# Kernel optimization log

Measured on AMD Instinct MI355X. Metric: run time of the kernel, lower is better.

The kernel has to match this reference:

```python
import jax, jax.numpy as jnp
import numpy as np

D = 256

def setup_inputs() -> dict:
    key = jax.random.key(0)
    k1, k2, k3, k4, k5, k6 = jax.random.split(key, 6)
    M, N = 2048, 512
    s = 1.0 / np.sqrt(D)
    return {
        "q_vec": jax.random.normal(k1, (M, D), dtype=jnp.float32),
        "kv": jax.random.normal(k2, (M, N, D), dtype=jnp.float32),
        "wq": jax.random.uniform(k3, (D, D), jnp.float32, -s, s),
        "wk": jax.random.uniform(k4, (D, D), jnp.float32, -s, s),
        "wv": jax.random.uniform(k5, (D, D), jnp.float32, -s, s),
        "wo": (jax.random.uniform(k6, (D, D), jnp.float32, -s, s)),
    }

def reference(q_vec, kv, wq, wk, wv, wo):
    # q_vec: [M, d], kv: [M, N, d]; weights stored torch-style [out, in] -> apply x @ W.T
    d = q_vec.shape[-1]
    q = q_vec @ wq.T                          # [M, d]
    k = jnp.einsum('mnd,ed->mne', kv, wk)     # [M, N, d]
    v = jnp.einsum('mnd,ed->mne', kv, wv)     # [M, N, d]
    logits = jnp.einsum('md,mnd->mn', q, k) / jnp.sqrt(jnp.float32(d))  # [M, N]
    attn = jax.nn.softmax(logits, axis=-1)    # [M, N] (dropout p=0.0 is identity)
    ctx = jnp.einsum('mn,mnd->md', attn, v)   # [M, d]
    out = ctx @ wo.T                          # [M, d]
    return out, attn
```

## Files before the change

kernel.cpp:

```cpp
#include <hip/hip_runtime.h>
#include <math.h>

#define DD 256
#define MM 2048
#define NN 512

typedef float f32x4 __attribute__((ext_vector_type(4)));

__device__ inline f32x4 ld_nt(const f32x4* p) { return __builtin_nontemporal_load(p); }

__global__ void prep_weights(const float* __restrict__ wq, const float* __restrict__ wk,
                             const float* __restrict__ wv, const float* __restrict__ wo,
                             float* __restrict__ W1, float* __restrict__ W2T) {
    __shared__ float sA[DD];
    const int j = threadIdx.x;
    const int b = blockIdx.x;
    if (b < DD) {
        const int d = b;
        sA[j] = wq[j * DD + d];
        __syncthreads();
        float acc = 0.f;
        for (int a = 0; a < DD; ++a) acc = fmaf(sA[a], wk[a * DD + j], acc);
        W1[d * DD + j] = acc * 0.0625f;
    } else {
        const int d = b - DD;
        sA[j] = wv[j * DD + d];
        __syncthreads();
        float acc = 0.f;
        for (int e = 0; e < DD; ++e) acc = fmaf(wo[j * DD + e], sA[e], acc);
        W2T[d * DD + j] = acc;
    }
}

template <int ROWS>
__global__ void rowgemm(const float* __restrict__ X, const float* __restrict__ W,
                        float* __restrict__ Y) {
    __shared__ float sX[ROWS][DD];
    const int j = threadIdx.x;
    const int m0 = blockIdx.x * ROWS;
    for (int r = 0; r < ROWS; ++r) sX[r][j] = X[(size_t)(m0 + r) * DD + j];
    __syncthreads();
    float acc[ROWS];
#pragma unroll
    for (int r = 0; r < ROWS; ++r) acc[r] = 0.f;
    for (int d = 0; d < DD; ++d) {
        const float w = W[d * DD + j];
#pragma unroll
        for (int r = 0; r < ROWS; ++r) acc[r] = fmaf(sX[r][d], w, acc[r]);
    }
    for (int r = 0; r < ROWS; ++r) Y[(size_t)(m0 + r) * DD + j] = acc[r];
}

__global__ __launch_bounds__(256, 4)
void attn_stream(const float* __restrict__ kv, const float* __restrict__ qt,
                 float* __restrict__ c_out, float* __restrict__ attn_out) {
    __shared__ float s_pe[NN];
    __shared__ float s_lw[4];
    __shared__ float s_wc[4][DD];
    __shared__ float s_qt[DD];

    const int m    = blockIdx.x;
    const int tid  = threadIdx.x;
    const int wave = tid >> 6;
    const int lane = tid & 63;
    const int grp  = lane >> 4;
    const int l16  = lane & 15;
    const int nbase = wave * 4 + grp;

    const f32x4* p = (const f32x4*)(kv + (size_t)m * NN * DD) + (size_t)nbase * 64 + l16;
    const int STRIDE = 16 * 64;

    f32x4 a0 = ld_nt(p), a1 = ld_nt(p + 16), a2 = ld_nt(p + 32), a3 = ld_nt(p + 48);

    s_qt[tid] = qt[(size_t)m * DD + tid];
    __syncthreads();

    const f32x4* qt4 = (const f32x4*)s_qt;
    const f32x4 qv0 = qt4[l16];
    const f32x4 qv1 = qt4[l16 + 16];
    const f32x4 qv2 = qt4[l16 + 32];
    const f32x4 qv3 = qt4[l16 + 48];

    f32x4 c0 = (f32x4)0.f, c1 = (f32x4)0.f, c2 = (f32x4)0.f, c3 = (f32x4)0.f;
    float lw = 0.f;

#pragma unroll 2
    for (int it = 0; it < NN / 16; ++it) {
        f32x4 b0, b1, b2, b3;
        if (it + 1 < NN / 16) {
            const f32x4* np = p + (size_t)(it + 1) * STRIDE;
            b0 = ld_nt(np); b1 = ld_nt(np + 16); b2 = ld_nt(np + 32); b3 = ld_nt(np + 48);
        }
        f32x4 t = a0 * qv0 + a1 * qv1 + a2 * qv2 + a3 * qv3;
        float pd = (t[0] + t[1]) + (t[2] + t[3]);
        pd += __shfl_xor(pd, 1);
        pd += __shfl_xor(pd, 2);
        pd += __shfl_xor(pd, 4);
        pd += __shfl_xor(pd, 8);

        const float pe = __expf(pd);
        if (l16 == 0) s_pe[it * 16 + nbase] = pe;
        lw += pe;

        c0 += pe * a0;
        c1 += pe * a1;
        c2 += pe * a2;
        c3 += pe * a3;

        a0 = b0; a1 = b1; a2 = b2; a3 = b3;
    }

#pragma unroll
    for (int i = 0; i < 4; ++i) {
        c0[i] += __shfl_xor(c0[i], 16); c1[i] += __shfl_xor(c1[i], 16);
        c2[i] += __shfl_xor(c2[i], 16); c3[i] += __shfl_xor(c3[i], 16);
        c0[i] += __shfl_xor(c0[i], 32); c1[i] += __shfl_xor(c1[i], 32);
        c2[i] += __shfl_xor(c2[i], 32); c3[i] += __shfl_xor(c3[i], 32);
    }
    lw += __shfl_xor(lw, 16);
    lw += __shfl_xor(lw, 32);

    {
        f32x4* wc4 = (f32x4*)(&s_wc[wave][0]);
        const f32x4 cg = (grp == 0) ? c0 : (grp == 1) ? c1 : (grp == 2) ? c2 : c3;
        wc4[grp * 16 + l16] = cg;
        if (lane == 0) s_lw[wave] = lw;
    }
    __syncthreads();

    const float L = (s_lw[0] + s_lw[1]) + (s_lw[2] + s_lw[3]);
    const float invL = 1.f / L;

    const float cd = ((s_wc[0][tid] + s_wc[1][tid]) + (s_wc[2][tid] + s_wc[3][tid])) * invL;
    c_out[(size_t)m * DD + tid] = cd;

    attn_out[(size_t)m * NN + tid]       = s_pe[tid] * invL;
    attn_out[(size_t)m * NN + tid + 256] = s_pe[tid + 256] * invL;
}

extern "C" void kernel_launch(void* const* d_in, const int* in_sizes, int n_in,
                              void* d_out, int out_size, void* d_ws, size_t ws_size,
                              hipStream_t stream) {
    const float* q_vec = (const float*)d_in[0];
    const float* kv    = (const float*)d_in[1];
    const float* wq    = (const float*)d_in[2];
    const float* wk    = (const float*)d_in[3];
    const float* wv    = (const float*)d_in[4];
    const float* wo    = (const float*)d_in[5];

    float* out  = (float*)d_out;
    float* attn = (float*)d_out + (size_t)MM * DD;

    float* W1  = (float*)d_ws;
    float* W2T = W1 + DD * DD;
    float* qt  = W2T + DD * DD;
    float* cws = qt + (size_t)MM * DD;

    prep_weights<<<2 * DD, DD, 0, stream>>>(wq, wk, wv, wo, W1, W2T);
    rowgemm<16><<<MM / 16, DD, 0, stream>>>(q_vec, W1, qt);
    attn_stream<<<MM, DD, 0, stream>>>(kv, qt, cws, attn);
    rowgemm<16><<<MM / 16, DD, 0, stream>>>(cws, W2T, out);
}
```

Measured before the change: 229.0 us.

## Fuse query and output projections into attention kernel; use packed FP32 FMA

```diff
diff --git a/kernel.cpp b/kernel.cpp
--- a/kernel.cpp
+++ b/kernel.cpp
@@ -6,8 +6,20 @@
 #define NN 512
 
 typedef float f32x4 __attribute__((ext_vector_type(4)));
+typedef float f32x2 __attribute__((ext_vector_type(2)));
 
 __device__ inline f32x4 ld_nt(const f32x4* p) { return __builtin_nontemporal_load(p); }
+
+__device__ inline void pk_fma(f32x2& d, f32x2 a, f32x2 b) {
+    asm("v_pk_fma_f32 %0, %1, %2, %0" : "+v"(d) : "v"(a), "v"(b));
+}
+__device__ inline f32x2 pk_mul(f32x2 a, f32x2 b) {
+    f32x2 d;
+    asm("v_pk_mul_f32 %0, %1, %2" : "=v"(d) : "v"(a), "v"(b));
+    return d;
+}
+__device__ inline f32x2 lo2(f32x4 v) { return __builtin_shufflevector(v, v, 0, 1); }
+__device__ inline f32x2 hi2(f32x4 v) { return __builtin_shufflevector(v, v, 2, 3); }
 
 __global__ void prep_weights(const float* __restrict__ wq, const float* __restrict__ wk,
                              const float* __restrict__ wv, const float* __restrict__ wo,
@@ -32,31 +44,14 @@
     }
 }
 
-template <int ROWS>
-__global__ void rowgemm(const float* __restrict__ X, const float* __restrict__ W,
-                        float* __restrict__ Y) {
-    __shared__ float sX[ROWS][DD];
-    const int j = threadIdx.x;
-    const int m0 = blockIdx.x * ROWS;
-    for (int r = 0; r < ROWS; ++r) sX[r][j] = X[(size_t)(m0 + r) * DD + j];
-    __syncthreads();
-    float acc[ROWS];
-#pragma unroll
-    for (int r = 0; r < ROWS; ++r) acc[r] = 0.f;
-    for (int d = 0; d < DD; ++d) {
-        const float w = W[d * DD + j];
-#pragma unroll
-        for (int r = 0; r < ROWS; ++r) acc[r] = fmaf(sX[r][d], w, acc[r]);
-    }
-    for (int r = 0; r < ROWS; ++r) Y[(size_t)(m0 + r) * DD + j] = acc[r];
-}
-
 __global__ __launch_bounds__(256, 4)
-void attn_stream(const float* __restrict__ kv, const float* __restrict__ qt,
-                 float* __restrict__ c_out, float* __restrict__ attn_out) {
+void attn_fused(const float* __restrict__ q_vec, const float* __restrict__ kv,
+                const float* __restrict__ W1, const float* __restrict__ W2T,
+                float* __restrict__ out, float* __restrict__ attn_out) {
     __shared__ float s_pe[NN];
     __shared__ float s_lw[4];
     __shared__ float s_wc[4][DD];
+    __shared__ float s_q[DD];
     __shared__ float s_qt[DD];
 
     const int m    = blockIdx.x;
@@ -67,22 +62,35 @@
     const int l16  = lane & 15;
     const int nbase = wave * 4 + grp;
 
+    s_q[tid] = q_vec[(size_t)m * DD + tid];
+    __syncthreads();
+    {
+        float a = 0.f;
+#pragma unroll 8
+        for (int d = 0; d < DD; ++d) a = fmaf(s_q[d], W1[d * DD + tid], a);
+        s_qt[tid] = a;
+    }
+    __syncthreads();
+
+    const f32x4* qt4 = (const f32x4*)s_qt;
+    f32x2 qp[8];
+    {
+        const f32x4 q0 = qt4[l16], q1 = qt4[l16 + 16], q2 = qt4[l16 + 32], q3 = qt4[l16 + 48];
+        qp[0] = lo2(q0); qp[1] = hi2(q0);
+        qp[2] = lo2(q1); qp[3] = hi2(q1);
+        qp[4] = lo2(q2); qp[5] = hi2(q2);
+        qp[6] = lo2(q3); qp[7] = hi2(q3);
+    }
+
     const f32x4* p = (const f32x4*)(kv + (size_t)m * NN * DD) + (size_t)nbase * 64 + l16;
     const int STRIDE = 16 * 64;
 
+    f32x2 cp[8];
+#pragma unroll
+    for (int i = 0; i < 8; ++i) cp[i] = (f32x2)0.f;
+    float lw = 0.f;
+
     f32x4 a0 = ld_nt(p), a1 = ld_nt(p + 16), a2 = ld_nt(p + 32), a3 = ld_nt(p + 48);
-
-    s_qt[tid] = qt[(size_t)m * DD + tid];
-    __syncthreads();
-
-    const f32x4* qt4 = (const f32x4*)s_qt;
-    const f32x4 qv0 = qt4[l16];
-    const f32x4 qv1 = qt4[l16 + 16];
-    const f32x4 qv2 = qt4[l16 + 32];
-    const f32x4 qv3 = qt4[l16 + 48];
-
-    f32x4 c0 = (f32x4)0.f, c1 = (f32x4)0.f, c2 = (f32x4)0.f, c3 = (f32x4)0.f;
-    float lw = 0.f;
 
 #pragma unroll 2
     for (int it = 0; it < NN / 16; ++it) {
@@ -91,8 +99,19 @@
             const f32x4* np = p + (size_t)(it + 1) * STRIDE;
             b0 = ld_nt(np); b1 = ld_nt(np + 16); b2 = ld_nt(np + 32); b3 = ld_nt(np + 48);
         }
-        f32x4 t = a0 * qv0 + a1 * qv1 + a2 * qv2 + a3 * qv3;
-        float pd = (t[0] + t[1]) + (t[2] + t[3]);
+
+        const f32x2 ap0 = lo2(a0), ap1 = hi2(a0), ap2 = lo2(a1), ap3 = hi2(a1);
+        const f32x2 ap4 = lo2(a2), ap5 = hi2(a2), ap6 = lo2(a3), ap7 = hi2(a3);
+
+        f32x2 t2 = pk_mul(ap0, qp[0]);
+        pk_fma(t2, ap1, qp[1]);
+        pk_fma(t2, ap2, qp[2]);
+        pk_fma(t2, ap3, qp[3]);
+        pk_fma(t2, ap4, qp[4]);
+        pk_fma(t2, ap5, qp[5]);
+        pk_fma(t2, ap6, qp[6]);
+        pk_fma(t2, ap7, qp[7]);
+        float pd = t2[0] + t2[1];
         pd += __shfl_xor(pd, 1);
         pd += __shfl_xor(pd, 2);
         pd += __shfl_xor(pd, 4);
@@ -102,28 +121,34 @@
         if (l16 == 0) s_pe[it * 16 + nbase] = pe;
         lw += pe;
 
-        c0 += pe * a0;
-        c1 += pe * a1;
-        c2 += pe * a2;
-        c3 += pe * a3;
+        f32x2 pe2; pe2[0] = pe; pe2[1] = pe;
+        pk_fma(cp[0], pe2, ap0);
+        pk_fma(cp[1], pe2, ap1);
+        pk_fma(cp[2], pe2, ap2);
+        pk_fma(cp[3], pe2, ap3);
+        pk_fma(cp[4], pe2, ap4);
+        pk_fma(cp[5], pe2, ap5);
+        pk_fma(cp[6], pe2, ap6);
+        pk_fma(cp[7], pe2, ap7);
 
         a0 = b0; a1 = b1; a2 = b2; a3 = b3;
     }
 
 #pragma unroll
-    for (int i = 0; i < 4; ++i) {
-        c0[i] += __shfl_xor(c0[i], 16); c1[i] += __shfl_xor(c1[i], 16);
-        c2[i] += __shfl_xor(c2[i], 16); c3[i] += __shfl_xor(c3[i], 16);
-        c0[i] += __shfl_xor(c0[i], 32); c1[i] += __shfl_xor(c1[i], 32);
-        c2[i] += __shfl_xor(c2[i], 32); c3[i] += __shfl_xor(c3[i], 32);
+    for (int i = 0; i < 8; ++i) {
+#pragma unroll
+        for (int j = 0; j < 2; ++j) {
+            cp[i][j] += __shfl_xor(cp[i][j], 16);
+            cp[i][j] += __shfl_xor(cp[i][j], 32);
+        }
     }
     lw += __shfl_xor(lw, 16);
     lw += __shfl_xor(lw, 32);
 
     {
-        f32x4* wc4 = (f32x4*)(&s_wc[wave][0]);
-        const f32x4 cg = (grp == 0) ? c0 : (grp == 1) ? c1 : (grp == 2) ? c2 : c3;
-        wc4[grp * 16 + l16] = cg;
+        f32x2* wc2 = (f32x2*)(&s_wc[wave][0]);
+        wc2[32 * grp + 2 * l16]     = cp[2 * grp];
+        wc2[32 * grp + 2 * l16 + 1] = cp[2 * grp + 1];
         if (lane == 0) s_lw[wave] = lw;
     }
     __syncthreads();
@@ -132,10 +157,17 @@
     const float invL = 1.f / L;
 
     const float cd = ((s_wc[0][tid] + s_wc[1][tid]) + (s_wc[2][tid] + s_wc[3][tid])) * invL;
-    c_out[(size_t)m * DD + tid] = cd;
+    __syncthreads();
+    s_q[tid] = cd;
+    __syncthreads();
 
     attn_out[(size_t)m * NN + tid]       = s_pe[tid] * invL;
     attn_out[(size_t)m * NN + tid + 256] = s_pe[tid + 256] * invL;
+
+    float o = 0.f;
+#pragma unroll 8
+    for (int d = 0; d < DD; ++d) o = fmaf(s_q[d], W2T[d * DD + tid], o);
+    out[(size_t)m * DD + tid] = o;
 }
 
 extern "C" void kernel_launch(void* const* d_in, const int* in_sizes, int n_in,
@@ -153,11 +185,7 @@
 
     float* W1  = (float*)d_ws;
     float* W2T = W1 + DD * DD;
-    float* qt  = W2T + DD * DD;
-    float* cws = qt + (size_t)MM * DD;
 
     prep_weights<<<2 * DD, DD, 0, stream>>>(wq, wk, wv, wo, W1, W2T);
-    rowgemm<16><<<MM / 16, DD, 0, stream>>>(q_vec, W1, qt);
-    attn_stream<<<MM, DD, 0, stream>>>(kv, qt, cws, attn);
-    rowgemm<16><<<MM / 16, DD, 0, stream>>>(cws, W2T, out);
+    attn_fused<<<MM, DD, 0, stream>>>(q_vec, kv, W1, W2T, out, attn);
 }
```

After: 216.0 us. -5.7%, faster.
